# Optimization experiments

Hardware: AMD Instinct MI355X
Metric: run time of the kernel (lower is better)

## Reference

```python
import jax, jax.numpy as jnp
import numpy as np

N_NODES = 100000
N_EDGES = 1000000
N_GRAPHS = 16
CUTOFF = 6.0
ETAS = [0.5, 1.0, 2.0, 4.0]
OFFSETS = [0.0, 1.0, 2.0, 3.0, 4.0, 5.0, 6.0, 7.0]
SPECIES = (0, 1, 2)


def setup_inputs() -> dict:
    key = jax.random.key(0)
    ks = jax.random.split(key, 6)
    pos = jax.random.normal(ks[0], (N_NODES, 3), dtype=jnp.float32)
    cell = jax.random.normal(ks[1], (N_GRAPHS, 3, 3), dtype=jnp.float32)
    edge_shift = jax.random.normal(ks[2], (N_EDGES, 3), dtype=jnp.float32)
    z = jax.random.randint(ks[3], (N_NODES,), 0, 3, dtype=jnp.int64)
    edge_index = jax.random.randint(ks[4], (2, N_EDGES), 0, N_NODES, dtype=jnp.int64)
    batch = jnp.sort(jax.random.randint(ks[5], (N_NODES,), 0, N_GRAPHS, dtype=jnp.int64))
    # buffers from torch.cartesian_prod(etas, offsets).t(): etas repeated, offsets tiled
    etas = jnp.repeat(jnp.asarray(ETAS, dtype=jnp.float32), len(OFFSETS))      # [P]
    offsets = jnp.tile(jnp.asarray(OFFSETS, dtype=jnp.float32), len(ETAS))     # [P]
    return {"pos": pos, "cell": cell, "edge_shift": edge_shift, "etas": etas,
            "offsets": offsets, "z": z, "edge_index": edge_index, "batch": batch}


def reference(pos, cell, edge_shift, etas, offsets, z, edge_index, batch):
    i = edge_index[0]  # receiver
    j = edge_index[1]  # sender
    # periodic-image-shifted edge vectors: [E,3]
    vec_ij = pos[j] - pos[i] + jnp.einsum('ni,nij->nj', edge_shift, cell[batch[i]])
    r_ij = jnp.linalg.norm(vec_ij, axis=-1)  # [E]
    # cosine cutoff
    fc = jnp.where(r_ij < CUTOFF, 0.5 * (jnp.cos(jnp.pi * r_ij / CUTOFF) + 1.0), 0.0)
    # Gaussian RBF per (eta, offset) pair: [P, E]
    G2_ij = jnp.exp(-etas[:, None] * (r_ij - offsets[:, None]) ** 2 / CUTOFF ** 2) * fc
    zj = z[j]
    outs = []
    for sp in SPECIES:  # small fixed loop over species (3)
        m = (zj == sp).astype(G2_ij.dtype)          # [E]
        seg = jax.ops.segment_sum((G2_ij * m).T, i, num_segments=pos.shape[0])  # [N, P]
        outs.append(seg.T)                           # [P, N]
    return jnp.concatenate(outs, axis=0)             # [S*P, N]
```

## Files before the change

kernel.cpp:

```cpp
#include <hip/hip_runtime.h>
#include <math.h>

#define N_NODES 100000
#define N_EDGES 1000000
#define NPAIR 32
#define CUTOFF 6.0f

#define CHUNK 512
#define NCHUNK ((N_NODES + CHUNK - 1) / CHUNK)
#define CAP 8192
#define K1_THREADS 1024
#define EPT 4
#define EPB (K1_THREADS * EPT)
#define K1_BLOCKS ((N_EDGES + EPB - 1) / EPB)
#define AT 512

__global__ __launch_bounds__(1024) void bin_kernel(
    const float* __restrict__ pos,
    const float* __restrict__ cell,
    const float* __restrict__ shift,
    const int*   __restrict__ z,
    const int*   __restrict__ ei,
    const int*   __restrict__ batch,
    unsigned int* __restrict__ bucket,
    int*          __restrict__ cur)
{
    __shared__ int lhist[NCHUNK];
    __shared__ int lbase[NCHUNK];
    int tid = threadIdx.x;

    if (tid < NCHUNK) lhist[tid] = 0;
    __syncthreads();

    int base = blockIdx.x * EPB;

    int iv[EPT], jv[EPT];
    float sx[EPT], sy[EPT], sz[EPT];
    bool val[EPT];
#pragma unroll
    for (int q = 0; q < EPT; ++q) {
        int e = base + tid + q * K1_THREADS;
        val[q] = (e < N_EDGES);
        int ee = val[q] ? e : 0;
        iv[q] = ei[ee];
        jv[q] = ei[N_EDGES + ee];
        sx[q] = shift[3 * ee + 0];
        sy[q] = shift[3 * ee + 1];
        sz[q] = shift[3 * ee + 2];
    }

    float pix[EPT], piy[EPT], piz[EPT], pjx[EPT], pjy[EPT], pjz[EPT];
    int zj[EPT], bi[EPT];
#pragma unroll
    for (int q = 0; q < EPT; ++q) {
        pix[q] = pos[3 * iv[q] + 0]; piy[q] = pos[3 * iv[q] + 1]; piz[q] = pos[3 * iv[q] + 2];
        pjx[q] = pos[3 * jv[q] + 0]; pjy[q] = pos[3 * jv[q] + 1]; pjz[q] = pos[3 * jv[q] + 2];
        zj[q] = z[jv[q]];
        bi[q] = batch[iv[q]];
    }

    unsigned int recs[EPT];
    int chks[EPT], locs[EPT];
#pragma unroll
    for (int q = 0; q < EPT; ++q) {
        chks[q] = -1;
        if (val[q]) {
            const float* C = cell + 9 * bi[q];
            float vx = pjx[q] - pix[q] + sx[q] * C[0] + sy[q] * C[3] + sz[q] * C[6];
            float vy = pjy[q] - piy[q] + sx[q] * C[1] + sy[q] * C[4] + sz[q] * C[7];
            float vz = pjz[q] - piz[q] + sx[q] * C[2] + sy[q] * C[5] + sz[q] * C[8];
            float r = sqrtf(vx * vx + vy * vy + vz * vz);
            if (r < CUTOFF) {
                unsigned int qq = (unsigned int)(r * (2097152.0f / 6.0f));
                qq = min(qq, 2097151u);
                int c = iv[q] >> 9;
                recs[q] = (qq << 11) | ((unsigned int)(iv[q] & 511) << 2)
                        | (unsigned int)(zj[q] & 3);
                chks[q] = c;
                locs[q] = atomicAdd(&lhist[c], 1);
            }
        }
    }
    __syncthreads();

    if (tid < NCHUNK) {
        int h  = lhist[tid];
        int hp = (h + 15) & ~15;
        lbase[tid] = (hp > 0) ? atomicAdd(&cur[tid * 16], hp) : 0;
    }
    __syncthreads();

#pragma unroll
    for (int q = 0; q < EPT; ++q) {
        if (chks[q] >= 0) {
            int slot = lbase[chks[q]] + locs[q];
            if (slot < CAP)
                bucket[(size_t)chks[q] * CAP + slot] = recs[q];
        }
    }

    if (tid < NCHUNK) {
        int h  = lhist[tid];
        int hp = (h + 15) & ~15;
        int b  = lbase[tid];
        for (int k = h; k < hp; ++k) {
            int slot = b + k;
            if (slot < CAP)
                bucket[(size_t)tid * CAP + slot] = 0xFFFFFFFFu;
        }
    }
}

__global__ __launch_bounds__(AT) void accum_kernel(
    const unsigned int* __restrict__ bucket,
    const int*          __restrict__ cur,
    float*              __restrict__ out)
{
    __shared__ unsigned int sorted[CAP];
    __shared__ int hist[CHUNK];
    __shared__ int lcur[CHUNK];
    int tid = threadIdx.x;
    int chunk = blockIdx.x;

    hist[tid] = 0;
    __syncthreads();

    int cnt = min(cur[chunk * 16], CAP);
    const unsigned int* b = bucket + (size_t)chunk * CAP;

    unsigned int regs[CAP / AT];
#pragma unroll
    for (int it = 0; it < CAP / AT; ++it) {
        int k = tid + it * AT;
        unsigned int rc = 0xFFFFFFFFu;
        if (k < cnt) rc = b[k];
        if ((rc & 3u) == 3u) rc = 0xFFFFFFFFu;
        else atomicAdd(&hist[(rc >> 2) & 511], 1);
        regs[it] = rc;
    }
    __syncthreads();

    int c0 = hist[tid];
    for (int d = 1; d < CHUNK; d <<= 1) {
        int y = (tid >= d) ? hist[tid - d] : 0;
        __syncthreads();
        hist[tid] += y;
        __syncthreads();
    }
    int incl = hist[tid];
    int beg  = incl - c0;
    lcur[tid] = beg;
    __syncthreads();

#pragma unroll
    for (int it = 0; it < CAP / AT; ++it) {
        unsigned int rc = regs[it];
        if (rc != 0xFFFFFFFFu) {
            int slot = atomicAdd(&lcur[(rc >> 2) & 511], 1);
            sorted[slot] = rc;
        }
    }
    __syncthreads();

    float a0[NPAIR], a1[NPAIR], a2[NPAIR];
#pragma unroll
    for (int p = 0; p < NPAIR; ++p) { a0[p] = 0.0f; a1[p] = 0.0f; a2[p] = 0.0f; }

    for (int k = beg; k < incl; ++k) {
        unsigned int rc = sorted[k];
        int spec = rc & 3;
        float r = (float)(rc >> 11) * (6.0f / 2097152.0f);
        float fc = 0.5f * (__cosf(r * (float)(M_PI / 6.0)) + 1.0f);
        float m0 = (spec == 0) ? fc : 0.0f;
        float m1 = (spec == 1) ? fc : 0.0f;
        float m2 = (spec == 2) ? fc : 0.0f;
#pragma unroll
        for (int o = 0; o < 8; ++o) {
            float d = r - (float)o;
            float e0 = __expf(d * d * (-0.5f / 36.0f));
            float e1 = e0 * e0;
            float e2 = e1 * e1;
            float e3 = e2 * e2;
            a0[o]      = fmaf(m0, e0, a0[o]);
            a1[o]      = fmaf(m1, e0, a1[o]);
            a2[o]      = fmaf(m2, e0, a2[o]);
            a0[8 + o]  = fmaf(m0, e1, a0[8 + o]);
            a1[8 + o]  = fmaf(m1, e1, a1[8 + o]);
            a2[8 + o]  = fmaf(m2, e1, a2[8 + o]);
            a0[16 + o] = fmaf(m0, e2, a0[16 + o]);
            a1[16 + o] = fmaf(m1, e2, a1[16 + o]);
            a2[16 + o] = fmaf(m2, e2, a2[16 + o]);
            a0[24 + o] = fmaf(m0, e3, a0[24 + o]);
            a1[24 + o] = fmaf(m1, e3, a1[24 + o]);
            a2[24 + o] = fmaf(m2, e3, a2[24 + o]);
        }
    }

    int node = chunk * CHUNK + tid;
    if (node < N_NODES) {
#pragma unroll
        for (int p = 0; p < NPAIR; ++p) {
            out[(size_t)(0 * NPAIR + p) * N_NODES + node] = a0[p];
            out[(size_t)(1 * NPAIR + p) * N_NODES + node] = a1[p];
            out[(size_t)(2 * NPAIR + p) * N_NODES + node] = a2[p];
        }
    }
}

extern "C" void kernel_launch(void* const* d_in, const int* in_sizes, int n_in,
                              void* d_out, int out_size, void* d_ws, size_t ws_size,
                              hipStream_t stream) {
    const float* pos   = (const float*)d_in[0];
    const float* cell  = (const float*)d_in[1];
    const float* shift = (const float*)d_in[2];
    const int*   z     = (const int*)d_in[5];
    const int*   ei    = (const int*)d_in[6];
    const int*   batch = (const int*)d_in[7];
    float* out = (float*)d_out;

    char* ws = (char*)d_ws;
    unsigned int* bucket = (unsigned int*)(ws);
    int*          cur    = (int*)(ws + (size_t)NCHUNK * CAP * 4);

    hipMemsetAsync(cur, 0, NCHUNK * 16 * sizeof(int), stream);

    bin_kernel<<<K1_BLOCKS, K1_THREADS, 0, stream>>>(pos, cell, shift, z, ei, batch,
                                                     bucket, cur);
    accum_kernel<<<NCHUNK, AT, 0, stream>>>(bucket, cur, out);
}
```

Baseline: 63.40 us.

## Pack node data into float4, split per-node accumulation across two threads

A new pack kernel stores pos, species and batch id for each node in one float4 and also zeroes the cursor array, replacing the memset. The edge binning kernel then does one vector gather per endpoint instead of several scalar gathers. The accumulation kernel now runs with 1024 threads, so two threads share each node's edges, and their partial sums are combined with a lane shuffle; output stores are split between the pair. This adds a launch and a packed buffer, and the shuffle-and-split adds some overhead in exchange for more parallelism in the exp-heavy accumulation loop.

```diff
diff --git a/kernel.cpp b/kernel.cpp
--- a/kernel.cpp
+++ b/kernel.cpp
@@ -7,21 +7,40 @@
 #define CUTOFF 6.0f
 
 #define CHUNK 512
-#define NCHUNK ((N_NODES + CHUNK - 1) / CHUNK)
+#define NCHUNK 196
 #define CAP 8192
 #define K1_THREADS 1024
 #define EPT 4
 #define EPB (K1_THREADS * EPT)
 #define K1_BLOCKS ((N_EDGES + EPB - 1) / EPB)
-#define AT 512
+#define AT 1024
+#define CURSTRIDE 16
+#define NCUR (NCHUNK * CURSTRIDE)
+
+__global__ __launch_bounds__(256) void pack_kernel(
+    const float* __restrict__ pos,
+    const int*   __restrict__ z,
+    const int*   __restrict__ batch,
+    float4*      __restrict__ packed,
+    int*         __restrict__ cur)
+{
+    int n = blockIdx.x * 256 + threadIdx.x;
+    if (n < NCUR) cur[n] = 0;
+    if (n < N_NODES) {
+        float4 p;
+        p.x = pos[3 * n + 0];
+        p.y = pos[3 * n + 1];
+        p.z = pos[3 * n + 2];
+        p.w = __int_as_float((z[n] & 3) | (batch[n] << 2));
+        packed[n] = p;
+    }
+}
 
 __global__ __launch_bounds__(1024) void bin_kernel(
-    const float* __restrict__ pos,
-    const float* __restrict__ cell,
-    const float* __restrict__ shift,
-    const int*   __restrict__ z,
-    const int*   __restrict__ ei,
-    const int*   __restrict__ batch,
+    const float4* __restrict__ packed,
+    const float*  __restrict__ cell,
+    const float*  __restrict__ shift,
+    const int*    __restrict__ ei,
     unsigned int* __restrict__ bucket,
     int*          __restrict__ cur)
 {
@@ -49,14 +68,11 @@
         sz[q] = shift[3 * ee + 2];
     }
 
-    float pix[EPT], piy[EPT], piz[EPT], pjx[EPT], pjy[EPT], pjz[EPT];
-    int zj[EPT], bi[EPT];
-#pragma unroll
-    for (int q = 0; q < EPT; ++q) {
-        pix[q] = pos[3 * iv[q] + 0]; piy[q] = pos[3 * iv[q] + 1]; piz[q] = pos[3 * iv[q] + 2];
-        pjx[q] = pos[3 * jv[q] + 0]; pjy[q] = pos[3 * jv[q] + 1]; pjz[q] = pos[3 * jv[q] + 2];
-        zj[q] = z[jv[q]];
-        bi[q] = batch[iv[q]];
+    float4 fi[EPT], fj[EPT];
+#pragma unroll
+    for (int q = 0; q < EPT; ++q) {
+        fi[q] = packed[iv[q]];
+        fj[q] = packed[jv[q]];
     }
 
     unsigned int recs[EPT];
@@ -65,17 +81,19 @@
     for (int q = 0; q < EPT; ++q) {
         chks[q] = -1;
         if (val[q]) {
-            const float* C = cell + 9 * bi[q];
-            float vx = pjx[q] - pix[q] + sx[q] * C[0] + sy[q] * C[3] + sz[q] * C[6];
-            float vy = pjy[q] - piy[q] + sx[q] * C[1] + sy[q] * C[4] + sz[q] * C[7];
-            float vz = pjz[q] - piz[q] + sx[q] * C[2] + sy[q] * C[5] + sz[q] * C[8];
+            int bi = __float_as_int(fi[q].w) >> 2;
+            int zj = __float_as_int(fj[q].w) & 3;
+            const float* C = cell + 9 * bi;
+            float vx = fj[q].x - fi[q].x + sx[q] * C[0] + sy[q] * C[3] + sz[q] * C[6];
+            float vy = fj[q].y - fi[q].y + sx[q] * C[1] + sy[q] * C[4] + sz[q] * C[7];
+            float vz = fj[q].z - fi[q].z + sx[q] * C[2] + sy[q] * C[5] + sz[q] * C[8];
             float r = sqrtf(vx * vx + vy * vy + vz * vz);
             if (r < CUTOFF) {
                 unsigned int qq = (unsigned int)(r * (2097152.0f / 6.0f));
                 qq = min(qq, 2097151u);
                 int c = iv[q] >> 9;
                 recs[q] = (qq << 11) | ((unsigned int)(iv[q] & 511) << 2)
-                        | (unsigned int)(zj[q] & 3);
+                        | (unsigned int)zj;
                 chks[q] = c;
                 locs[q] = atomicAdd(&lhist[c], 1);
             }
@@ -86,7 +104,7 @@
     if (tid < NCHUNK) {
         int h  = lhist[tid];
         int hp = (h + 15) & ~15;
-        lbase[tid] = (hp > 0) ? atomicAdd(&cur[tid * 16], hp) : 0;
+        lbase[tid] = (hp > 0) ? atomicAdd(&cur[tid * CURSTRIDE], hp) : 0;
     }
     __syncthreads();
 
@@ -122,10 +140,10 @@
     int tid = threadIdx.x;
     int chunk = blockIdx.x;
 
-    hist[tid] = 0;
-    __syncthreads();
-
-    int cnt = min(cur[chunk * 16], CAP);
+    if (tid < CHUNK) hist[tid] = 0;
+    __syncthreads();
+
+    int cnt = min(cur[chunk * CURSTRIDE], CAP);
     const unsigned int* b = bucket + (size_t)chunk * CAP;
 
     unsigned int regs[CAP / AT];
@@ -140,16 +158,15 @@
     }
     __syncthreads();
 
-    int c0 = hist[tid];
+    int c0 = (tid < CHUNK) ? hist[tid] : 0;
     for (int d = 1; d < CHUNK; d <<= 1) {
-        int y = (tid >= d) ? hist[tid - d] : 0;
+        int y = 0;
+        if (tid < CHUNK && tid >= d) y = hist[tid - d];
         __syncthreads();
-        hist[tid] += y;
+        if (tid < CHUNK) hist[tid] += y;
         __syncthreads();
     }
-    int incl = hist[tid];
-    int beg  = incl - c0;
-    lcur[tid] = beg;
+    if (tid < CHUNK) lcur[tid] = hist[tid] - c0;
     __syncthreads();
 
 #pragma unroll
@@ -162,11 +179,16 @@
     }
     __syncthreads();
 
+    int node_loc = tid >> 1;
+    int par = tid & 1;
+    int s_beg = (node_loc > 0) ? hist[node_loc - 1] : 0;
+    int incl = hist[node_loc];
+
     float a0[NPAIR], a1[NPAIR], a2[NPAIR];
 #pragma unroll
     for (int p = 0; p < NPAIR; ++p) { a0[p] = 0.0f; a1[p] = 0.0f; a2[p] = 0.0f; }
 
-    for (int k = beg; k < incl; ++k) {
+    for (int k = s_beg + par; k < incl; k += 2) {
         unsigned int rc = sorted[k];
         int spec = rc & 3;
         float r = (float)(rc >> 11) * (6.0f / 2097152.0f);
@@ -196,13 +218,29 @@
         }
     }
 
-    int node = chunk * CHUNK + tid;
+#pragma unroll
+    for (int p = 0; p < NPAIR; ++p) {
+        a0[p] += __shfl_xor(a0[p], 1);
+        a1[p] += __shfl_xor(a1[p], 1);
+        a2[p] += __shfl_xor(a2[p], 1);
+    }
+
+    int node = chunk * CHUNK + node_loc;
     if (node < N_NODES) {
-#pragma unroll
-        for (int p = 0; p < NPAIR; ++p) {
-            out[(size_t)(0 * NPAIR + p) * N_NODES + node] = a0[p];
-            out[(size_t)(1 * NPAIR + p) * N_NODES + node] = a1[p];
-            out[(size_t)(2 * NPAIR + p) * N_NODES + node] = a2[p];
+        if (par == 0) {
+#pragma unroll
+            for (int p = 0; p < NPAIR; ++p)
+                out[(size_t)p * N_NODES + node] = a0[p];
+#pragma unroll
+            for (int p = 0; p < 16; ++p)
+                out[(size_t)(NPAIR + p) * N_NODES + node] = a1[p];
+        } else {
+#pragma unroll
+            for (int p = 16; p < NPAIR; ++p)
+                out[(size_t)(NPAIR + p) * N_NODES + node] = a1[p];
+#pragma unroll
+            for (int p = 0; p < NPAIR; ++p)
+                out[(size_t)(2 * NPAIR + p) * N_NODES + node] = a2[p];
         }
     }
 }
@@ -220,11 +258,13 @@
 
     char* ws = (char*)d_ws;
     unsigned int* bucket = (unsigned int*)(ws);
-    int*          cur    = (int*)(ws + (size_t)NCHUNK * CAP * 4);
-
-    hipMemsetAsync(cur, 0, NCHUNK * 16 * sizeof(int), stream);
-
-    bin_kernel<<<K1_BLOCKS, K1_THREADS, 0, stream>>>(pos, cell, shift, z, ei, batch,
+    int*          cur    = (int*)(ws + 6422528);
+    float4*       packed = (float4*)(ws + 6435072);
+
+    int pblocks = (N_NODES + 255) / 256;
+    pack_kernel<<<pblocks, 256, 0, stream>>>(pos, z, batch, packed, cur);
+
+    bin_kernel<<<K1_BLOCKS, K1_THREADS, 0, stream>>>(packed, cell, shift, ei,
                                                      bucket, cur);
     accum_kernel<<<NCHUNK, AT, 0, stream>>>(bucket, cur, out);
 }
```

New measurement: 76.89 us. 21.3% more time.

## Replace global atomic bucketing with per-block fixed slices and per-node LDS bins

Applied to the files above, without the earlier changes.

The binning kernel now writes records into fixed per-(chunk, block) slices of 31 entries plus a count word, which removes the global atomic cursor, the memset and the padding writes. The accumulation kernel splits each chunk into two half-blocks. Each one reads all slices with uint4 loads and scatters records into per-node LDS bins capped at 32 entries, so the prefix-scan sort is no longer needed. The cost is that every accum block reads the whole chunk's slices, and records are silently dropped if a block slice overflows 31 or a node has more than 32 neighbors. At roughly 10 edges per node with about 10 expected per slice, both caps are rarely exceeded.

```diff
diff --git a/kernel.cpp b/kernel.cpp
--- a/kernel.cpp
+++ b/kernel.cpp
@@ -7,39 +7,45 @@
 #define CUTOFF 6.0f
 
 #define CHUNK 512
-#define NCHUNK ((N_NODES + CHUNK - 1) / CHUNK)
-#define CAP 8192
-#define K1_THREADS 1024
-#define EPT 4
-#define EPB (K1_THREADS * EPT)
-#define K1_BLOCKS ((N_EDGES + EPB - 1) / EPB)
-#define AT 512
+#define NCHUNK 196
+#define HALF 256
 
-__global__ __launch_bounds__(1024) void bin_kernel(
+#define NT_BIN 256
+#define EPT 8
+#define EPB (NT_BIN * EPT)
+#define NB_BIN ((N_EDGES + EPB - 1) / EPB)
+
+#define SLICE 32
+#define PAYLOAD 31
+#define NODECAP 32
+#define BSTRIDE 33
+
+#define NB_ACC (NCHUNK * 2)
+
+__global__ __launch_bounds__(NT_BIN, 2) void bin_kernel(
     const float* __restrict__ pos,
     const float* __restrict__ cell,
     const float* __restrict__ shift,
     const int*   __restrict__ z,
     const int*   __restrict__ ei,
     const int*   __restrict__ batch,
-    unsigned int* __restrict__ bucket,
-    int*          __restrict__ cur)
+    unsigned int* __restrict__ bucket)
 {
     __shared__ int lhist[NCHUNK];
-    __shared__ int lbase[NCHUNK];
     int tid = threadIdx.x;
+    int blk = blockIdx.x;
 
     if (tid < NCHUNK) lhist[tid] = 0;
     __syncthreads();
 
-    int base = blockIdx.x * EPB;
+    int base = blk * EPB;
 
     int iv[EPT], jv[EPT];
     float sx[EPT], sy[EPT], sz[EPT];
     bool val[EPT];
 #pragma unroll
     for (int q = 0; q < EPT; ++q) {
-        int e = base + tid + q * K1_THREADS;
+        int e = base + tid + q * NT_BIN;
         val[q] = (e < N_EDGES);
         int ee = val[q] ? e : 0;
         iv[q] = ei[ee];
@@ -59,11 +65,8 @@
         bi[q] = batch[iv[q]];
     }
 
-    unsigned int recs[EPT];
-    int chks[EPT], locs[EPT];
 #pragma unroll
     for (int q = 0; q < EPT; ++q) {
-        chks[q] = -1;
         if (val[q]) {
             const float* C = cell + 9 * bi[q];
             float vx = pjx[q] - pix[q] + sx[q] * C[0] + sy[q] * C[3] + sz[q] * C[6];
@@ -74,100 +77,69 @@
                 unsigned int qq = (unsigned int)(r * (2097152.0f / 6.0f));
                 qq = min(qq, 2097151u);
                 int c = iv[q] >> 9;
-                recs[q] = (qq << 11) | ((unsigned int)(iv[q] & 511) << 2)
-                        | (unsigned int)(zj[q] & 3);
-                chks[q] = c;
-                locs[q] = atomicAdd(&lhist[c], 1);
+                unsigned int rec = (qq << 11) | ((unsigned int)(iv[q] & 511) << 2)
+                                 | (unsigned int)(zj[q] & 3);
+                int loc = atomicAdd(&lhist[c], 1);
+                if (loc < PAYLOAD)
+                    bucket[((size_t)c * NB_BIN + blk) * SLICE + loc] = rec;
             }
         }
     }
     __syncthreads();
 
     if (tid < NCHUNK) {
-        int h  = lhist[tid];
-        int hp = (h + 15) & ~15;
-        lbase[tid] = (hp > 0) ? atomicAdd(&cur[tid * 16], hp) : 0;
-    }
-    __syncthreads();
-
-#pragma unroll
-    for (int q = 0; q < EPT; ++q) {
-        if (chks[q] >= 0) {
-            int slot = lbase[chks[q]] + locs[q];
-            if (slot < CAP)
-                bucket[(size_t)chks[q] * CAP + slot] = recs[q];
-        }
-    }
-
-    if (tid < NCHUNK) {
-        int h  = lhist[tid];
-        int hp = (h + 15) & ~15;
-        int b  = lbase[tid];
-        for (int k = h; k < hp; ++k) {
-            int slot = b + k;
-            if (slot < CAP)
-                bucket[(size_t)tid * CAP + slot] = 0xFFFFFFFFu;
-        }
+        unsigned int h = (unsigned int)min(lhist[tid], PAYLOAD);
+        bucket[((size_t)tid * NB_BIN + blk) * SLICE + PAYLOAD] = h;
     }
 }
 
-__global__ __launch_bounds__(AT) void accum_kernel(
+__global__ __launch_bounds__(256, 2) void accum_kernel(
     const unsigned int* __restrict__ bucket,
-    const int*          __restrict__ cur,
     float*              __restrict__ out)
 {
-    __shared__ unsigned int sorted[CAP];
-    __shared__ int hist[CHUNK];
-    __shared__ int lcur[CHUNK];
+    __shared__ unsigned int bins[HALF * BSTRIDE];
+    __shared__ int lcur[HALF];
+    __shared__ int scnt[NB_BIN];
     int tid = threadIdx.x;
-    int chunk = blockIdx.x;
+    int chunk = blockIdx.x >> 1;
+    int half  = blockIdx.x & 1;
+    int locbase = half * HALF;
 
-    hist[tid] = 0;
+    lcur[tid] = 0;
+    for (int s = tid; s < NB_BIN; s += 256)
+        scnt[s] = (int)bucket[((size_t)chunk * NB_BIN + s) * SLICE + PAYLOAD];
     __syncthreads();
 
-    int cnt = min(cur[chunk * 16], CAP);
-    const unsigned int* b = bucket + (size_t)chunk * CAP;
+    const uint4* b4 = (const uint4*)(bucket + (size_t)chunk * NB_BIN * SLICE);
+    const int n4 = NB_BIN * (SLICE / 4);
 
-    unsigned int regs[CAP / AT];
+    for (int k = tid; k < n4; k += 256) {
+        uint4 v = b4[k];
+        int s  = k >> 3;
+        int w0 = (k & 7) << 2;
+        int cnt = scnt[s];
+        unsigned int rr[4] = {v.x, v.y, v.z, v.w};
 #pragma unroll
-    for (int it = 0; it < CAP / AT; ++it) {
-        int k = tid + it * AT;
-        unsigned int rc = 0xFFFFFFFFu;
-        if (k < cnt) rc = b[k];
-        if ((rc & 3u) == 3u) rc = 0xFFFFFFFFu;
-        else atomicAdd(&hist[(rc >> 2) & 511], 1);
-        regs[it] = rc;
-    }
-    __syncthreads();
-
-    int c0 = hist[tid];
-    for (int d = 1; d < CHUNK; d <<= 1) {
-        int y = (tid >= d) ? hist[tid - d] : 0;
-        __syncthreads();
-        hist[tid] += y;
-        __syncthreads();
-    }
-    int incl = hist[tid];
-    int beg  = incl - c0;
-    lcur[tid] = beg;
-    __syncthreads();
-
-#pragma unroll
-    for (int it = 0; it < CAP / AT; ++it) {
-        unsigned int rc = regs[it];
-        if (rc != 0xFFFFFFFFu) {
-            int slot = atomicAdd(&lcur[(rc >> 2) & 511], 1);
-            sorted[slot] = rc;
+        for (int u = 0; u < 4; ++u) {
+            if (w0 + u < cnt) {
+                unsigned int rc = rr[u];
+                int l = (int)((rc >> 2) & 511) - locbase;
+                if ((unsigned)l < HALF) {
+                    int slot = atomicAdd(&lcur[l], 1);
+                    if (slot < NODECAP) bins[l * BSTRIDE + slot] = rc;
+                }
+            }
         }
     }
     __syncthreads();
 
+    int n = min(lcur[tid], NODECAP);
     float a0[NPAIR], a1[NPAIR], a2[NPAIR];
 #pragma unroll
     for (int p = 0; p < NPAIR; ++p) { a0[p] = 0.0f; a1[p] = 0.0f; a2[p] = 0.0f; }
 
-    for (int k = beg; k < incl; ++k) {
-        unsigned int rc = sorted[k];
+    for (int k = 0; k < n; ++k) {
+        unsigned int rc = bins[tid * BSTRIDE + k];
         int spec = rc & 3;
         float r = (float)(rc >> 11) * (6.0f / 2097152.0f);
         float fc = 0.5f * (__cosf(r * (float)(M_PI / 6.0)) + 1.0f);
@@ -196,7 +168,7 @@
         }
     }
 
-    int node = chunk * CHUNK + tid;
+    int node = chunk * CHUNK + locbase + tid;
     if (node < N_NODES) {
 #pragma unroll
         for (int p = 0; p < NPAIR; ++p) {
@@ -218,13 +190,8 @@
     const int*   batch = (const int*)d_in[7];
     float* out = (float*)d_out;
 
-    char* ws = (char*)d_ws;
-    unsigned int* bucket = (unsigned int*)(ws);
-    int*          cur    = (int*)(ws + (size_t)NCHUNK * CAP * 4);
+    unsigned int* bucket = (unsigned int*)d_ws;
 
-    hipMemsetAsync(cur, 0, NCHUNK * 16 * sizeof(int), stream);
-
-    bin_kernel<<<K1_BLOCKS, K1_THREADS, 0, stream>>>(pos, cell, shift, z, ei, batch,
-                                                     bucket, cur);
-    accum_kernel<<<NCHUNK, AT, 0, stream>>>(bucket, cur, out);
+    bin_kernel<<<NB_BIN, NT_BIN, 0, stream>>>(pos, cell, shift, z, ei, batch, bucket);
+    accum_kernel<<<NB_ACC, 256, 0, stream>>>(bucket, out);
 }
```

Result: faster. 57.93 us (-8.6%).
